# Kernel optimization log

Measured on AMD Instinct MI355X. Metric: run time of the kernel, lower is better.

The kernel has to match this reference:

```python
import jax, jax.numpy as jnp
import numpy as np

B, T, D = 8, 1024, 768
H = 12
DH = D // H
FF = 3072
EPS = 1e-12


def setup_inputs() -> dict:
    key = jax.random.key(0)
    ks = jax.random.split(key, 12)
    s = 0.02
    return {
        "x": jax.random.normal(ks[0], (B, T, D), dtype=jnp.float32),
        "Wq": jax.random.normal(ks[1], (D, D), dtype=jnp.float32) * s,
        "Wk": jax.random.normal(ks[2], (D, D), dtype=jnp.float32) * s,
        "Wv": jax.random.normal(ks[3], (D, D), dtype=jnp.float32) * s,
        "Wo": jax.random.normal(ks[4], (D, D), dtype=jnp.float32) * s,
        "bo": jnp.zeros((D,), dtype=jnp.float32),
        "W1": jax.random.normal(ks[5], (FF, D), dtype=jnp.float32) * s,
        "b1": jnp.zeros((FF,), dtype=jnp.float32),
        "W2": jax.random.normal(ks[6], (D, FF), dtype=jnp.float32) * s,
        "b2": jnp.zeros((D,), dtype=jnp.float32),
        "ln1_w": jnp.ones((D,), dtype=jnp.float32),
        "ln1_b": jnp.zeros((D,), dtype=jnp.float32),
        "ln2_w": jnp.ones((D,), dtype=jnp.float32),
        "ln2_b": jnp.zeros((D,), dtype=jnp.float32),
    }


def _layer_norm(x, w, b, eps=EPS):
    mu = jnp.mean(x, axis=-1, keepdims=True)
    var = jnp.mean((x - mu) ** 2, axis=-1, keepdims=True)
    return (x - mu) * jax.lax.rsqrt(var + eps) * w + b


def _self_attn(x, Wq, Wk, Wv, Wo, bo):
    # x: [B, T, D]; q/k/v projections are bias-free (F.linear with weight only)
    q = (x @ Wq.T).reshape(B, T, H, DH)
    k = (x @ Wk.T).reshape(B, T, H, DH)
    v = (x @ Wv.T).reshape(B, T, H, DH)
    scale = 1.0 / np.sqrt(DH).astype(np.float32)
    scores = jnp.einsum("bqhd,bkhd->bhqk", q, k) * scale  # [B,H,T,T]
    attn = jax.nn.softmax(scores, axis=-1)
    o = jnp.einsum("bhqk,bkhd->bqhd", attn, v).reshape(B, T, D)
    return o @ Wo.T + bo


def reference(x, Wq, Wk, Wv, Wo, bo, W1, b1, W2, b2, ln1_w, ln1_b, ln2_w, ln2_b):
    # Pre-norm ViT encoder block (dropout = 0 / eval mode)
    h = x + _self_attn(_layer_norm(x, ln1_w, ln1_b), Wq, Wk, Wv, Wo, bo)
    z = _layer_norm(h, ln2_w, ln2_b)
    ff = jax.nn.gelu(z @ W1.T + b1, approximate=False) @ W2.T + b2
    return h + ff
```

## Files before the change

### kernel.cpp

```cpp
#include <hip/hip_runtime.h>
#include <hip/hip_bf16.h>
#include <math.h>

#define CB 8
#define CT 1024
#define CD 768
#define CH 12
#define CDH 64
#define CFF 3072
#define CBT 8192

typedef unsigned short u16;
typedef __attribute__((ext_vector_type(8))) short bf16x8;
typedef __attribute__((ext_vector_type(4))) float f32x4;
typedef __attribute__((address_space(1))) unsigned int gu32;
typedef __attribute__((address_space(3))) unsigned int su32;

__device__ __forceinline__ u16 f2bf(float f) {
  union { float f; unsigned u; } v; v.f = f;
  unsigned r = v.u + 0x7fffu + ((v.u >> 16) & 1u);
  return (u16)(r >> 16);
}

__device__ __forceinline__ void gload16(const u16* g, u16* l) {
  __builtin_amdgcn_global_load_lds((gu32*)g, (su32*)l, 16, 0, 0);
}

__device__ __forceinline__ float gelu_f(float x) {
  float y = 0.7978845608028654f * (x + 0.044715f * x * x * x);
  float t = 1.f - 2.f / (__expf(2.f * y) + 1.f);
  return 0.5f * x * (1.f + t);
}

__global__ __launch_bounds__(256) void cvt_bf16(const float* __restrict__ in,
                                                u16* __restrict__ out, int n) {
  int i = blockIdx.x * 256 + threadIdx.x;
  if (i < n) out[i] = f2bf(in[i]);
}

__global__ __launch_bounds__(256) void ln_kernel(const float* __restrict__ X,
                                                 const float* __restrict__ gw,
                                                 const float* __restrict__ gb,
                                                 u16* __restrict__ Y) {
  __shared__ float red[4];
  const int row = blockIdx.x, tid = threadIdx.x;
  const float* xr = X + (size_t)row * CD;
  float v0 = xr[tid], v1 = xr[tid + 256], v2 = xr[tid + 512];
  float s = v0 + v1 + v2;
#pragma unroll
  for (int o = 32; o > 0; o >>= 1) s += __shfl_down(s, o);
  if ((tid & 63) == 0) red[tid >> 6] = s;
  __syncthreads();
  float mu = (red[0] + red[1] + red[2] + red[3]) * (1.f / 768.f);
  __syncthreads();
  float d0 = v0 - mu, d1 = v1 - mu, d2 = v2 - mu;
  float q = d0 * d0 + d1 * d1 + d2 * d2;
#pragma unroll
  for (int o = 32; o > 0; o >>= 1) q += __shfl_down(q, o);
  if ((tid & 63) == 0) red[tid >> 6] = q;
  __syncthreads();
  float var = (red[0] + red[1] + red[2] + red[3]) * (1.f / 768.f);
  float rstd = rsqrtf(var + 1e-12f);
  u16* yr = Y + (size_t)row * CD;
  yr[tid]       = f2bf(d0 * rstd * gw[tid]       + gb[tid]);
  yr[tid + 256] = f2bf(d1 * rstd * gw[tid + 256] + gb[tid + 256]);
  yr[tid + 512] = f2bf(d2 * rstd * gw[tid + 512] + gb[tid + 512]);
}

template <int ACT, int BIAS, int RES, int OMODE>
__global__ __launch_bounds__(256, 4) void gemm_bt(
    const u16* __restrict__ A, const u16* __restrict__ Bt,
    const float* __restrict__ bias, const float* __restrict__ res,
    void* __restrict__ outp, u16* __restrict__ vtp, int M, int N, int K) {
  __shared__ __align__(16) u16 Asm[128 * 64];
  __shared__ __align__(16) u16 Bsm[128 * 64];
  const int tid = threadIdx.x;
  const int gx = gridDim.x;
  const int nwg = gx * gridDim.y;
  const int wg = blockIdx.y * gx + blockIdx.x;
  const int swz = (wg & 7) * (nwg >> 3) + (wg >> 3);
  const int bx = swz % gx, by = swz / gx;
  const int brow = by * 128, bcol = bx * 128;
  const int w = tid >> 6, l = tid & 63;
  const int wm = w >> 1, wn = w & 1;
  const int lr = l & 15, g = l >> 4;
  const f32x4 zf = {0.f, 0.f, 0.f, 0.f};
  f32x4 acc[4][4];
#pragma unroll
  for (int i = 0; i < 4; ++i)
#pragma unroll
    for (int j = 0; j < 4; ++j) acc[i][j] = zf;

  auto stage = [&](int kk) {
#pragma unroll
    for (int rr = 0; rr < 4; ++rr) {
      int c = rr * 256 + tid;
      int row = c >> 3, ch = c & 7;
      int sch = ch ^ (row & 7);
      gload16(A + (size_t)(brow + row) * K + kk + sch * 8, &Asm[(c & ~63) * 8]);
      gload16(Bt + (size_t)(bcol + row) * K + kk + sch * 8, &Bsm[(c & ~63) * 8]);
    }
  };

  const int NT = K >> 6;
  for (int t = 0; t < NT; ++t) {
    stage(t << 6);
    __syncthreads();
    bf16x8 af[4][2], bfr[4][2];
#pragma unroll
    for (int mi = 0; mi < 4; ++mi) {
      const int R = wm * 64 + mi * 16 + lr;
#pragma unroll
      for (int k2 = 0; k2 < 2; ++k2)
        af[mi][k2] = *(const bf16x8*)&Asm[R * 64 + (((k2 * 4 + g) ^ (R & 7)) * 8)];
    }
#pragma unroll
    for (int ni = 0; ni < 4; ++ni) {
      const int R = wn * 64 + ni * 16 + lr;
#pragma unroll
      for (int k2 = 0; k2 < 2; ++k2)
        bfr[ni][k2] = *(const bf16x8*)&Bsm[R * 64 + (((k2 * 4 + g) ^ (R & 7)) * 8)];
    }
#pragma unroll
    for (int k2 = 0; k2 < 2; ++k2)
#pragma unroll
      for (int mi = 0; mi < 4; ++mi)
#pragma unroll
        for (int ni = 0; ni < 4; ++ni)
          acc[mi][ni] = __builtin_amdgcn_mfma_f32_16x16x32_bf16(
              af[mi][k2], bfr[ni][k2], acc[mi][ni], 0, 0, 0);
    __syncthreads();
  }
#pragma unroll
  for (int mi = 0; mi < 4; ++mi) {
#pragma unroll
    for (int ni = 0; ni < 4; ++ni) {
      const int col = bcol + wn * 64 + ni * 16 + lr;
      float bv = 0.f;
      if (BIAS) bv = bias[col];
#pragma unroll
      for (int r = 0; r < 4; ++r) {
        const int row = brow + wm * 64 + mi * 16 + g * 4 + r;
        float v = acc[mi][ni][r] + bv;
        if (ACT == 1) v = gelu_f(v);
        if (RES) v += res[(size_t)row * N + col];
        if (OMODE == 0) {
          ((float*)outp)[(size_t)row * N + col] = v;
        } else if (OMODE == 1) {
          ((u16*)outp)[(size_t)row * N + col] = f2bf(v);
        } else {
          if (bcol < 2 * CD) {
            ((u16*)outp)[(size_t)row * (2 * CD) + col] = f2bf(v);
          } else {
            int vc = col - 2 * CD;
            int hI = vc >> 6, dI = vc & 63;
            int bI = row >> 10, tI = row & 1023;
            vtp[((size_t)((bI * CH + hI) * 64 + dI)) * CT + tI] = f2bf(v);
          }
        }
      }
    }
  }
}

__global__ __launch_bounds__(256) void attn_fa(const u16* __restrict__ QK,
                                               const u16* __restrict__ Vt,
                                               u16* __restrict__ O) {
  __shared__ __align__(16) u16 Ksm[2][64 * 64];
  __shared__ __align__(16) u16 Vsm[2][64 * 64];
  __shared__ __align__(16) u16 Psm[4 * 32 * 64];
  const int LDQ = 2 * CD;
  const int tid = threadIdx.x;
  const int w = tid >> 6, l = tid & 63;
  const int lr = l & 15, g = l >> 4;
  const int wg = (blockIdx.z * CH + blockIdx.y) * 8 + blockIdx.x;
  const int swzid = (wg & 7) * 96 + (wg >> 3);
  const int qb = (swzid & 7) * 128;
  const int rem = swzid >> 3;
  const int hh = rem % CH;
  const int bb = rem / CH;
  const size_t rowb = (size_t)bb * CT;
  const int hc = hh * CDH;
  const u16* Qp = QK;
  const u16* Kp = QK + CD;
  const size_t vbase = (size_t)((bb * CH + hh) * 64) * CT;

  bf16x8 qA0, qA1, qB0, qB1;
  {
    const u16* qr = Qp + (rowb + qb + w * 32 + lr) * LDQ + hc;
    qA0 = *(const bf16x8*)(qr + g * 8);
    qA1 = *(const bf16x8*)(qr + 32 + g * 8);
    const u16* qr2 = qr + 16 * LDQ;
    qB0 = *(const bf16x8*)(qr2 + g * 8);
    qB1 = *(const bf16x8*)(qr2 + 32 + g * 8);
  }
  const f32x4 zf = {0.f, 0.f, 0.f, 0.f};
  f32x4 oA[4], oB[4];
#pragma unroll
  for (int i = 0; i < 4; ++i) { oA[i] = zf; oB[i] = zf; }
  float lsA[4] = {0.f, 0.f, 0.f, 0.f};
  float lsB[4] = {0.f, 0.f, 0.f, 0.f};
  u16* Pw = Psm + w * (32 * 64);

  auto stage = [&](int buf, int kt) {
#pragma unroll
    for (int rr = 0; rr < 2; ++rr) {
      int c = rr * 256 + tid;
      int trow = c >> 3, tch = c & 7;
      int sch = tch ^ (trow & 7);
      gload16(Kp + (rowb + kt + trow) * LDQ + hc + sch * 8, &Ksm[buf][(c & ~63) * 8]);
      gload16(Vt + vbase + (size_t)trow * CT + kt + sch * 8, &Vsm[buf][(c & ~63) * 8]);
    }
  };

  stage(0, 0);
  __syncthreads();
  for (int t = 0; t < CT / 64; ++t) {
    const int cur = t & 1;
    if (t + 1 < CT / 64) stage(cur ^ 1, (t + 1) * 64);
#pragma unroll
    for (int ni = 0; ni < 4; ++ni) {
      const int krow = (ni * 16 + lr) * 64;
      bf16x8 kf0 = *(const bf16x8*)&Ksm[cur][krow + ((g ^ (lr & 7)) * 8)];
      bf16x8 kf1 = *(const bf16x8*)&Ksm[cur][krow + (((4 + g) ^ (lr & 7)) * 8)];
      f32x4 zA = zf, zB = zf;
      zA = __builtin_amdgcn_mfma_f32_16x16x32_bf16(qA0, kf0, zA, 0, 0, 0);
      zA = __builtin_amdgcn_mfma_f32_16x16x32_bf16(qA1, kf1, zA, 0, 0, 0);
      zB = __builtin_amdgcn_mfma_f32_16x16x32_bf16(qB0, kf0, zB, 0, 0, 0);
      zB = __builtin_amdgcn_mfma_f32_16x16x32_bf16(qB1, kf1, zB, 0, 0, 0);
      const int pcol = ni * 2 + (lr >> 3);
#pragma unroll
      for (int r = 0; r < 4; ++r) {
        const int prow = g * 4 + r;
        float pA = __expf(zA[r] * 0.125f);
        float pB = __expf(zB[r] * 0.125f);
        lsA[r] += pA;
        lsB[r] += pB;
        const int sw = ((pcol ^ (prow & 7)) << 3) + (lr & 7);
        Pw[prow * 64 + sw] = f2bf(pA);
        Pw[(prow + 16) * 64 + sw] = f2bf(pB);
      }
    }
#pragma unroll
    for (int ks = 0; ks < 2; ++ks) {
      const int pch = (((ks * 4 + g) ^ (lr & 7)) << 3);
      bf16x8 pfA = *(const bf16x8*)&Pw[lr * 64 + pch];
      bf16x8 pfB = *(const bf16x8*)&Pw[(16 + lr) * 64 + pch];
#pragma unroll
      for (int ni = 0; ni < 4; ++ni) {
        bf16x8 vf = *(const bf16x8*)&Vsm[cur][(ni * 16 + lr) * 64 + pch];
        oA[ni] = __builtin_amdgcn_mfma_f32_16x16x32_bf16(pfA, vf, oA[ni], 0, 0, 0);
        oB[ni] = __builtin_amdgcn_mfma_f32_16x16x32_bf16(pfB, vf, oB[ni], 0, 0, 0);
      }
    }
    __syncthreads();
  }
#pragma unroll
  for (int o = 8; o > 0; o >>= 1)
#pragma unroll
    for (int r = 0; r < 4; ++r) {
      lsA[r] += __shfl_xor(lsA[r], o);
      lsB[r] += __shfl_xor(lsB[r], o);
    }
  float invA[4], invB[4];
#pragma unroll
  for (int r = 0; r < 4; ++r) {
    invA[r] = 1.f / lsA[r];
    invB[r] = 1.f / lsB[r];
  }
#pragma unroll
  for (int ni = 0; ni < 4; ++ni)
#pragma unroll
    for (int r = 0; r < 4; ++r) {
      const size_t rA = rowb + qb + w * 32 + g * 4 + r;
      O[rA * CD + hc + ni * 16 + lr] = f2bf(oA[ni][r] * invA[r]);
      O[(rA + 16) * CD + hc + ni * 16 + lr] = f2bf(oB[ni][r] * invB[r]);
    }
}

extern "C" void kernel_launch(void* const* d_in, const int* in_sizes, int n_in,
                              void* d_out, int out_size, void* d_ws, size_t ws_size,
                              hipStream_t stream) {
  (void)in_sizes; (void)n_in; (void)out_size; (void)ws_size;
  const float* x    = (const float*)d_in[0];
  const float* Wq   = (const float*)d_in[1];
  const float* Wk   = (const float*)d_in[2];
  const float* Wv   = (const float*)d_in[3];
  const float* Wo   = (const float*)d_in[4];
  const float* bo   = (const float*)d_in[5];
  const float* W1   = (const float*)d_in[6];
  const float* b1   = (const float*)d_in[7];
  const float* W2   = (const float*)d_in[8];
  const float* b2   = (const float*)d_in[9];
  const float* ln1w = (const float*)d_in[10];
  const float* ln1b = (const float*)d_in[11];
  const float* ln2w = (const float*)d_in[12];
  const float* ln2b = (const float*)d_in[13];
  float* out = (float*)d_out;

  char* ws = (char*)d_ws;
  size_t off = 0;
  auto alloc = [&](size_t bytes) -> char* {
    char* p = ws + off;
    off += (bytes + 255) & ~(size_t)255;
    return p;
  };
  u16* wqkv = (u16*)alloc((size_t)3 * CD * CD * 2);
  u16* wob  = (u16*)alloc((size_t)CD * CD * 2);
  u16* w1b  = (u16*)alloc((size_t)CFF * CD * 2);
  u16* w2b  = (u16*)alloc((size_t)CD * CFF * 2);
  u16* xn   = (u16*)alloc((size_t)CBT * CD * 2);
  u16* qk   = (u16*)alloc((size_t)CBT * 2 * CD * 2);
  u16* vt   = (u16*)alloc((size_t)CBT * CD * 2);
  float* hb = (float*)alloc((size_t)CBT * CD * 4);
  u16* ff1  = (u16*)alloc((size_t)CBT * CFF * 2);

  u16* attnb = xn;
  u16* zb = qk;

  const int DD = CD * CD;
  const int DF = CD * CFF;
  cvt_bf16<<<dim3((DD + 255) / 256), dim3(256), 0, stream>>>(Wq, wqkv, DD);
  cvt_bf16<<<dim3((DD + 255) / 256), dim3(256), 0, stream>>>(Wk, wqkv + DD, DD);
  cvt_bf16<<<dim3((DD + 255) / 256), dim3(256), 0, stream>>>(Wv, wqkv + 2 * DD, DD);
  cvt_bf16<<<dim3((DD + 255) / 256), dim3(256), 0, stream>>>(Wo, wob, DD);
  cvt_bf16<<<dim3((DF + 255) / 256), dim3(256), 0, stream>>>(W1, w1b, DF);
  cvt_bf16<<<dim3((DF + 255) / 256), dim3(256), 0, stream>>>(W2, w2b, DF);

  ln_kernel<<<dim3(CBT), dim3(256), 0, stream>>>(x, ln1w, ln1b, xn);

  gemm_bt<0, 0, 0, 2><<<dim3(3 * CD / 128, CBT / 128), dim3(256), 0, stream>>>(
      xn, wqkv, nullptr, nullptr, qk, vt, CBT, 3 * CD, CD);

  attn_fa<<<dim3(CT / 128, CH, CB), dim3(256), 0, stream>>>(qk, vt, attnb);

  gemm_bt<0, 1, 1, 0><<<dim3(CD / 128, CBT / 128), dim3(256), 0, stream>>>(
      attnb, wob, bo, x, hb, nullptr, CBT, CD, CD);

  ln_kernel<<<dim3(CBT), dim3(256), 0, stream>>>(hb, ln2w, ln2b, zb);

  gemm_bt<1, 1, 0, 1><<<dim3(CFF / 128, CBT / 128), dim3(256), 0, stream>>>(
      zb, w1b, b1, nullptr, ff1, nullptr, CBT, CFF, CD);

  gemm_bt<0, 1, 1, 0><<<dim3(CD / 128, CBT / 128), dim3(256), 0, stream>>>(
      ff1, w2b, b2, hb, out, nullptr, CBT, CD, CFF);
}
```

Measured before the change: 266.5 us.

## Merge weight conversions, store residual h in bf16, raise GEMM occupancy

Replaces six weight-conversion launches with one combined kernel. Stores the intermediate residual h as bf16 instead of fp32, so the out-projection GEMM writes fewer bytes and both LN2 and the final GEMM's residual read fewer. Raises the GEMM launch-bounds minimum blocks from 4 to 5. Rounding the residual to bf16 costs accuracy in the final output, and the occupancy hint may cause register spills.

```diff
diff --git a/kernel.cpp b/kernel.cpp
--- a/kernel.cpp
+++ b/kernel.cpp
@@ -22,6 +22,11 @@
   return (u16)(r >> 16);
 }
 
+__device__ __forceinline__ float bf2f(u16 u) {
+  union { unsigned u; float f; } v; v.u = ((unsigned)u) << 16;
+  return v.f;
+}
+
 __device__ __forceinline__ void gload16(const u16* g, u16* l) {
   __builtin_amdgcn_global_load_lds((gu32*)g, (su32*)l, 16, 0, 0);
 }
@@ -32,20 +37,38 @@
   return 0.5f * x * (1.f + t);
 }
 
-__global__ __launch_bounds__(256) void cvt_bf16(const float* __restrict__ in,
-                                                u16* __restrict__ out, int n) {
+__global__ __launch_bounds__(256) void cvt_all(
+    const float* __restrict__ Wq, const float* __restrict__ Wk,
+    const float* __restrict__ Wv, const float* __restrict__ Wo,
+    const float* __restrict__ W1, const float* __restrict__ W2,
+    u16* __restrict__ wqkv, u16* __restrict__ wob,
+    u16* __restrict__ w1b, u16* __restrict__ w2b) {
+  const int DD = CD * CD;
+  const int DF = CD * CFF;
   int i = blockIdx.x * 256 + threadIdx.x;
-  if (i < n) out[i] = f2bf(in[i]);
-}
-
-__global__ __launch_bounds__(256) void ln_kernel(const float* __restrict__ X,
+  if (i < DD)                wqkv[i] = f2bf(Wq[i]);
+  else if (i < 2 * DD)       wqkv[i] = f2bf(Wk[i - DD]);
+  else if (i < 3 * DD)       wqkv[i] = f2bf(Wv[i - 2 * DD]);
+  else if (i < 4 * DD)       wob[i - 3 * DD] = f2bf(Wo[i - 3 * DD]);
+  else if (i < 4 * DD + DF)  w1b[i - 4 * DD] = f2bf(W1[i - 4 * DD]);
+  else if (i < 4 * DD + 2 * DF) w2b[i - 4 * DD - DF] = f2bf(W2[i - 4 * DD - DF]);
+}
+
+template <int INBF>
+__global__ __launch_bounds__(256) void ln_kernel(const void* __restrict__ Xv,
                                                  const float* __restrict__ gw,
                                                  const float* __restrict__ gb,
                                                  u16* __restrict__ Y) {
   __shared__ float red[4];
   const int row = blockIdx.x, tid = threadIdx.x;
-  const float* xr = X + (size_t)row * CD;
-  float v0 = xr[tid], v1 = xr[tid + 256], v2 = xr[tid + 512];
+  float v0, v1, v2;
+  if (INBF) {
+    const u16* xr = (const u16*)Xv + (size_t)row * CD;
+    v0 = bf2f(xr[tid]); v1 = bf2f(xr[tid + 256]); v2 = bf2f(xr[tid + 512]);
+  } else {
+    const float* xr = (const float*)Xv + (size_t)row * CD;
+    v0 = xr[tid]; v1 = xr[tid + 256]; v2 = xr[tid + 512];
+  }
   float s = v0 + v1 + v2;
 #pragma unroll
   for (int o = 32; o > 0; o >>= 1) s += __shfl_down(s, o);
@@ -68,9 +91,9 @@
 }
 
 template <int ACT, int BIAS, int RES, int OMODE>
-__global__ __launch_bounds__(256, 4) void gemm_bt(
+__global__ __launch_bounds__(256, 5) void gemm_bt(
     const u16* __restrict__ A, const u16* __restrict__ Bt,
-    const float* __restrict__ bias, const float* __restrict__ res,
+    const float* __restrict__ bias, const void* __restrict__ res,
     void* __restrict__ outp, u16* __restrict__ vtp, int M, int N, int K) {
   __shared__ __align__(16) u16 Asm[128 * 64];
   __shared__ __align__(16) u16 Bsm[128 * 64];
@@ -143,7 +166,8 @@
         const int row = brow + wm * 64 + mi * 16 + g * 4 + r;
         float v = acc[mi][ni][r] + bv;
         if (ACT == 1) v = gelu_f(v);
-        if (RES) v += res[(size_t)row * N + col];
+        if (RES == 1) v += ((const float*)res)[(size_t)row * N + col];
+        if (RES == 2) v += bf2f(((const u16*)res)[(size_t)row * N + col]);
         if (OMODE == 0) {
           ((float*)outp)[(size_t)row * N + col] = v;
         } else if (OMODE == 1) {
@@ -312,36 +336,31 @@
   u16* xn   = (u16*)alloc((size_t)CBT * CD * 2);
   u16* qk   = (u16*)alloc((size_t)CBT * 2 * CD * 2);
   u16* vt   = (u16*)alloc((size_t)CBT * CD * 2);
-  float* hb = (float*)alloc((size_t)CBT * CD * 4);
+  u16* hbb  = (u16*)alloc((size_t)CBT * CD * 2);
   u16* ff1  = (u16*)alloc((size_t)CBT * CFF * 2);
 
   u16* attnb = xn;
   u16* zb = qk;
 
-  const int DD = CD * CD;
-  const int DF = CD * CFF;
-  cvt_bf16<<<dim3((DD + 255) / 256), dim3(256), 0, stream>>>(Wq, wqkv, DD);
-  cvt_bf16<<<dim3((DD + 255) / 256), dim3(256), 0, stream>>>(Wk, wqkv + DD, DD);
-  cvt_bf16<<<dim3((DD + 255) / 256), dim3(256), 0, stream>>>(Wv, wqkv + 2 * DD, DD);
-  cvt_bf16<<<dim3((DD + 255) / 256), dim3(256), 0, stream>>>(Wo, wob, DD);
-  cvt_bf16<<<dim3((DF + 255) / 256), dim3(256), 0, stream>>>(W1, w1b, DF);
-  cvt_bf16<<<dim3((DF + 255) / 256), dim3(256), 0, stream>>>(W2, w2b, DF);
-
-  ln_kernel<<<dim3(CBT), dim3(256), 0, stream>>>(x, ln1w, ln1b, xn);
+  const int NW = 4 * CD * CD + 2 * CD * CFF;
+  cvt_all<<<dim3((NW + 255) / 256), dim3(256), 0, stream>>>(
+      Wq, Wk, Wv, Wo, W1, W2, wqkv, wob, w1b, w2b);
+
+  ln_kernel<0><<<dim3(CBT), dim3(256), 0, stream>>>(x, ln1w, ln1b, xn);
 
   gemm_bt<0, 0, 0, 2><<<dim3(3 * CD / 128, CBT / 128), dim3(256), 0, stream>>>(
       xn, wqkv, nullptr, nullptr, qk, vt, CBT, 3 * CD, CD);
 
   attn_fa<<<dim3(CT / 128, CH, CB), dim3(256), 0, stream>>>(qk, vt, attnb);
 
-  gemm_bt<0, 1, 1, 0><<<dim3(CD / 128, CBT / 128), dim3(256), 0, stream>>>(
-      attnb, wob, bo, x, hb, nullptr, CBT, CD, CD);
-
-  ln_kernel<<<dim3(CBT), dim3(256), 0, stream>>>(hb, ln2w, ln2b, zb);
+  gemm_bt<0, 1, 1, 1><<<dim3(CD / 128, CBT / 128), dim3(256), 0, stream>>>(
+      attnb, wob, bo, x, hbb, nullptr, CBT, CD, CD);
+
+  ln_kernel<1><<<dim3(CBT), dim3(256), 0, stream>>>(hbb, ln2w, ln2b, zb);
 
   gemm_bt<1, 1, 0, 1><<<dim3(CFF / 128, CBT / 128), dim3(256), 0, stream>>>(
       zb, w1b, b1, nullptr, ff1, nullptr, CBT, CFF, CD);
 
-  gemm_bt<0, 1, 1, 0><<<dim3(CD / 128, CBT / 128), dim3(256), 0, stream>>>(
-      ff1, w2b, b2, hb, out, nullptr, CBT, CD, CFF);
-}
+  gemm_bt<0, 1, 2, 0><<<dim3(CD / 128, CBT / 128), dim3(256), 0, stream>>>(
+      ff1, w2b, b2, hbb, out, nullptr, CBT, CD, CFF);
+}
```

Measured after the change: 410.8 us. 54.2% more time.
